# Kernel tuning notes

Measured on AMD Instinct MI355X. Metric: run time of the kernel, lower is better.

The kernel has to match this reference:

```python
import jax, jax.numpy as jnp
import numpy as np

BUCKET = 32   # bucket_size hard-coded in module
HEADS = 8
LN_EPS = 1e-5
SELF_ATTN_VALUE = -5e4  # TOKEN_SELF_ATTN_VALUE from reformer-pytorch


def _layer_norm(x, g, b):
    m = jnp.mean(x, axis=-1, keepdims=True)
    v = jnp.mean((x - m) ** 2, axis=-1, keepdims=True)
    return (x - m) / jnp.sqrt(v + LN_EPS) * g + b


def _lsh_attention(qk, v, rot):
    # qk, v: (B=b*h, T, Dh); rot: (Dh, n_buckets//2); n_hashes = 1
    B, T, D = qk.shape
    n_buckets = T // BUCKET
    # hash: random rotations, argmax over [r, -r]
    r = jnp.einsum('btf,fi->bti', qk, rot)                 # (B, T, n_buckets//2)
    r = jnp.concatenate([r, -r], axis=-1)                  # (B, T, n_buckets)
    buckets = jnp.argmax(r, axis=-1)                       # (B, T) int
    t = jnp.arange(T)
    key = buckets * T + t                                  # unique sort key
    sticker = jnp.argsort(key, axis=-1)                    # (B, T) permutation
    undo = jnp.argsort(sticker, axis=-1)
    sqk = jnp.take_along_axis(qk, sticker[..., None], axis=1)
    sv = jnp.take_along_axis(v, sticker[..., None], axis=1)
    # chunk into n_buckets chunks of size BUCKET
    bq_t = sticker.reshape(B, n_buckets, BUCKET)
    bq = sqk.reshape(B, n_buckets, BUCKET, D)
    bv = sv.reshape(B, n_buckets, BUCKET, D)
    nrm = jnp.sqrt(jnp.sum(bq * bq, axis=-1, keepdims=True))
    bk = bq / jnp.maximum(nrm, 1e-12)                      # shared-QK: keys are unit-norm queries
    def look_one_back(xx):
        return jnp.concatenate([xx, jnp.roll(xx, 1, axis=1)], axis=2)
    bk = look_one_back(bk)
    bvv = look_one_back(bv)
    bkv_t = look_one_back(bq_t)
    dots = jnp.einsum('bcie,bcje->bcij', bq, bk) * (D ** -0.5)  # (B, C, 32, 64)
    self_mask = bq_t[:, :, :, None] == bkv_t[:, :, None, :]
    dots = jnp.where(self_mask, SELF_ATTN_VALUE, dots)
    attn = jax.nn.softmax(dots, axis=-1)
    bo = jnp.einsum('bcij,bcje->bcie', attn, bvv)
    so = bo.reshape(B, T, D)
    return jnp.take_along_axis(so, undo[..., None], axis=1)   # unsort (n_hashes=1 -> probs=1)


def _lsh_self_attention(h, w_qk, w_v, w_out, b_out, rot):
    b, t, d = h.shape
    dh = d // HEADS
    qk = (h @ w_qk).reshape(b, t, HEADS, dh).transpose(0, 2, 1, 3).reshape(b * HEADS, t, dh)
    vv = (h @ w_v).reshape(b, t, HEADS, dh).transpose(0, 2, 1, 3).reshape(b * HEADS, t, dh)
    o = _lsh_attention(qk, vv, rot)
    o = o.reshape(b, HEADS, t, dh).transpose(0, 2, 1, 3).reshape(b, t, d)
    return o @ w_out + b_out


def setup_inputs() -> dict:
    key = jax.random.key(0)
    ks = jax.random.split(key, 8)
    B, T, D, F = 8, 4096, 512, 2048
    dh, nb = D // HEADS, T // BUCKET
    s = 0.02
    return {
        'x': jax.random.normal(ks[0], (B, T, D), jnp.float32),
        'w_qk': jax.random.normal(ks[1], (D, D), jnp.float32) * s,
        'w_v': jax.random.normal(ks[2], (D, D), jnp.float32) * s,
        'w_out': jax.random.normal(ks[3], (D, D), jnp.float32) * s,
        'b_out': jnp.zeros((D,), jnp.float32),
        'ln1_g': jnp.ones((D,), jnp.float32),
        'ln1_b': jnp.zeros((D,), jnp.float32),
        'w_ff1': jax.random.normal(ks[4], (D, F), jnp.float32) * s,
        'b_ff1': jnp.zeros((F,), jnp.float32),
        'w_ff2': jax.random.normal(ks[5], (F, D), jnp.float32) * s,
        'b_ff2': jnp.zeros((D,), jnp.float32),
        'ln2_g': jnp.ones((D,), jnp.float32),
        'ln2_b': jnp.zeros((D,), jnp.float32),
        'rotations': jax.random.normal(ks[6], (dh, nb // 2), jnp.float32),
    }


def reference(x, w_qk, w_v, w_out, b_out, ln1_g, ln1_b, w_ff1, b_ff1,
              w_ff2, b_ff2, ln2_g, ln2_b, rotations):
    # y1 = x + Attn(LN1(x)); y2 = x + FFN(LN2(y1)); out = mean(y1, y2)
    h1 = _layer_norm(x, ln1_g, ln1_b)
    y1 = x + _lsh_self_attention(h1, w_qk, w_v, w_out, b_out, rotations)
    h2 = _layer_norm(y1, ln2_g, ln2_b)
    ffn = jax.nn.relu(h2 @ w_ff1 + b_ff1) @ w_ff2 + b_ff2
    y2 = x + ffn
    return 0.5 * (y1 + y2)
```

## Files before the change

### kernel.cpp

```cpp
#include <hip/hip_runtime.h>
#include <stdint.h>

typedef _Float16 f16;
typedef _Float16 f16x8 __attribute__((ext_vector_type(8)));
typedef float    f32x4 __attribute__((ext_vector_type(4)));
typedef unsigned long long u64;

__device__ __forceinline__ void gload16(const void* g, void* l) {
  __builtin_amdgcn_global_load_lds(
      (__attribute__((address_space(1))) void*)g,
      (__attribute__((address_space(3))) void*)l, 16, 0, 0);
}

#define MFMA_QUAD(q, af) \
  _Pragma("unroll") for (int m2 = 0; m2 < 2; ++m2) \
  _Pragma("unroll") for (int nt = 0; nt < 4; ++nt) \
  _Pragma("unroll") for (int kk = 0; kk < 2; ++kk) \
    acc[(q)*2 + m2][nt] = __builtin_amdgcn_mfma_f32_16x16x32_f16( \
        af[m2][kk], bf[nt][kk], acc[(q)*2 + m2][nt], 0, 0, 0);

#define RD_A(dst, abase, q2) \
  _Pragma("unroll") for (int m2 = 0; m2 < 2; ++m2) \
  _Pragma("unroll") for (int kk = 0; kk < 2; ++kk) { \
    const int lr = (q2)*32 + m2*16 + l15; \
    dst[m2][kk] = *(const f16x8*)&abase[lr*64 + (((kk*4 + l4) ^ (lr & 7)) << 3)]; }

#define RD_B(bbase) \
  _Pragma("unroll") for (int nt = 0; nt < 4; ++nt) \
  _Pragma("unroll") for (int kk = 0; kk < 2; ++kk) { \
    const int lr = brow + nt*16 + l15; \
    bf[nt][kk] = *(const f16x8*)&bbase[lr*64 + (((kk*4 + l4) ^ (lr & 7)) << 3)]; }

#define PH_PRE() \
  __builtin_amdgcn_s_barrier(); \
  asm volatile("s_waitcnt lgkmcnt(0)" ::: "memory"); \
  __builtin_amdgcn_sched_barrier(0); \
  __builtin_amdgcn_s_setprio(1);

#define PH_POST() \
  __builtin_amdgcn_s_setprio(0); \
  __builtin_amdgcn_s_barrier(); \
  __builtin_amdgcn_sched_barrier(0);

template<int EPI>
__global__ __launch_bounds__(512, 2)
void gemm256(const f16* __restrict__ A, int lda,
             const f16* __restrict__ Bt, int ldb,
             int K, int N,
             float* __restrict__ outf, f16* __restrict__ outh,
             f16* __restrict__ outh2,
             const float* __restrict__ bias,
             const float* __restrict__ add1)
{
  __shared__ __align__(16) f16 lds[65536];
  const int tid = threadIdx.x, lane = tid & 63;
  const int wid = tid >> 6;
  const int wm = wid >> 2, wn = wid & 3;
  const int l15 = lane & 15, l4 = lane >> 4;

  const int gx = gridDim.x;
  int lid = blockIdx.y * gx + blockIdx.x;
  const int cpx = (gx * gridDim.y) >> 3;
  lid = (lid & 7) * cpx + (lid >> 3);
  const long bm0 = (long)(lid / gx) * 256;
  const long bn0 = (long)(lid % gx) * 256;

  const int rs = tid >> 3, cs = tid & 7;
  const int cg = cs ^ (rs & 7);
  const int nkt = K >> 6;
  const int nmask = nkt - 1;

  auto stageA = [&](int d, int half, int kt) {
    f16* dst = &lds[(d * 4 + half) * 8192];
    const long kb = (long)kt * 64 + cg * 8;
    const f16* src = A + (bm0 + half * 128) * lda + kb;
#pragma unroll
    for (int rr = 0; rr < 2; ++rr) {
      const int row = rs + rr * 64;
      gload16(src + (long)row * lda, dst + row * 64 + cs * 8);
    }
  };
  auto stageB = [&](int d, int half, int kt) {
    f16* dst = &lds[(d * 4 + 2 + half) * 8192];
    const long kb = (long)kt * 64 + cg * 8;
    const f16* src = Bt + (bn0 + half * 128) * ldb + kb;
#pragma unroll
    for (int rr = 0; rr < 2; ++rr) {
      const int row = rs + rr * 64;
      gload16(src + (long)row * ldb, dst + row * 64 + cs * 8);
    }
  };

  const f16* aBase0 = &lds[(0 + wm) * 8192];
  const f16* aBase1 = &lds[(4 + wm) * 8192];
  const f16* bBase0 = &lds[(2 + (wn >> 1)) * 8192];
  const f16* bBase1 = &lds[(6 + (wn >> 1)) * 8192];
  const int brow = (wn & 1) * 64;

  f32x4 acc[8][4];
#pragma unroll
  for (int i = 0; i < 8; ++i)
#pragma unroll
    for (int j = 0; j < 4; ++j) acc[i][j] = f32x4{0.f, 0.f, 0.f, 0.f};
  f16x8 bf[4][2], afA[2][2], afB[2][2];

  stageB(0, 0, 0); stageB(0, 1, 0); stageA(0, 0, 0); stageA(0, 1, 0);
  asm volatile("s_waitcnt vmcnt(4)" ::: "memory");
  stageB(1, 0, 1); stageB(1, 1, 1); stageA(1, 0, 1);
  asm volatile("s_waitcnt vmcnt(6)" ::: "memory");
  __builtin_amdgcn_s_barrier();
  __builtin_amdgcn_sched_barrier(0);

  for (int j = 0; j < nkt; j += 2) {
    const int t2 = (j + 2) & nmask, t3 = (j + 3) & nmask;
    RD_B(bBase0); RD_A(afA, aBase0, 0);
    stageA(1, 1, (j + 1) & nmask);
    asm volatile("s_waitcnt lgkmcnt(8)" ::: "memory");
    PH_PRE(); MFMA_QUAD(0, afA); PH_POST();
    RD_A(afB, aBase0, 1); RD_A(afA, aBase0, 2);
    stageB(0, 0, t2);
    PH_PRE(); MFMA_QUAD(1, afB); PH_POST();
    RD_A(afB, aBase0, 3);
    stageB(0, 1, t2);
    PH_PRE(); MFMA_QUAD(2, afA); PH_POST();
    stageA(0, 0, t2);
    asm volatile("s_waitcnt vmcnt(6)" ::: "memory");
    PH_PRE(); MFMA_QUAD(3, afB); PH_POST();
    RD_B(bBase1); RD_A(afA, aBase1, 0);
    stageA(0, 1, t2);
    asm volatile("s_waitcnt lgkmcnt(8)" ::: "memory");
    PH_PRE(); MFMA_QUAD(0, afA); PH_POST();
    RD_A(afB, aBase1, 1); RD_A(afA, aBase1, 2);
    stageB(1, 0, t3);
    PH_PRE(); MFMA_QUAD(1, afB); PH_POST();
    RD_A(afB, aBase1, 3);
    stageB(1, 1, t3);
    PH_PRE(); MFMA_QUAD(2, afA); PH_POST();
    stageA(1, 0, t3);
    asm volatile("s_waitcnt vmcnt(6)" ::: "memory");
    PH_PRE(); MFMA_QUAD(3, afB); PH_POST();
  }
  asm volatile("s_waitcnt vmcnt(0)" ::: "memory");

#pragma unroll
  for (int mt = 0; mt < 8; ++mt)
#pragma unroll
    for (int nt = 0; nt < 4; ++nt)
#pragma unroll
      for (int r = 0; r < 4; ++r) {
        const long grow = bm0 + wm * 128 + mt * 16 + l4 * 4 + r;
        const long gcol = bn0 + wn * 64 + nt * 16 + l15;
        const float c = acc[mt][nt][r];
        if constexpr (EPI == 12) {
          const long idx = grow * (long)N + gcol;
          outf[idx] = c + bias[gcol] + add1[idx];
        } else if constexpr (EPI == 13) {
          const long idx = grow * (long)N + gcol;
          outh[idx] = (f16)fmaxf(c + bias[gcol], 0.f);
        } else if constexpr (EPI == 17) {
          const int bb = (int)(grow >> 12), tt = (int)(grow & 4095);
          const int hcol = (int)(bn0 >> 6) + wn;
          const int is_v = hcol >> 3, h = hcol & 7;
          f16* base = is_v ? outh2 : outh;
          base[(((long)bb * 8 + h) * 4096 + tt) * 64 + nt * 16 + l15] = (f16)c;
        }
      }
}

__global__ __launch_bounds__(512)
void gemm8_ffn2(const f16* __restrict__ A,
                const f16* __restrict__ Bt,
                const f16* __restrict__ sxyh,
                const float* __restrict__ bias,
                float* __restrict__ outf)
{
  __shared__ __align__(16) f16 sA[128 * 64];
  __shared__ __align__(16) f16 sB[128 * 64];
  const int tid  = threadIdx.x;
  const int lane = tid & 63;
  const int wv   = tid >> 6;
  const int wm   = wv >> 2, wn = wv & 3;
  const int l15  = lane & 15, l4 = lane >> 4;

  const int gx = gridDim.x;
  int lid = blockIdx.y * gx + blockIdx.x;
  const int cpx = (gx * gridDim.y) >> 3;
  lid = (lid & 7) * cpx + (lid >> 3);
  const long bm0 = (long)(lid / gx) * 128;
  const long bn0 = (long)(lid % gx) * 128;

  f32x4 acc[4][2];
#pragma unroll
  for (int i = 0; i < 4; ++i)
#pragma unroll
    for (int j = 0; j < 2; ++j) acc[i][j] = f32x4{0.f, 0.f, 0.f, 0.f};

  const int rs = tid >> 3;
  const int cs = tid & 7;
  const int cg = cs ^ (rs & 7);

  for (int kt = 0; kt < 32; ++kt) {
    __syncthreads();
    const long ka = (long)kt * 64 + cg * 8;
#pragma unroll
    for (int rd = 0; rd < 2; ++rd) {
      const int row = rs + rd * 64;
      gload16(A + (bm0 + row) * 2048 + ka, &sA[row * 64 + cs * 8]);
    }
#pragma unroll
    for (int rd = 0; rd < 2; ++rd) {
      const int row = rs + rd * 64;
      gload16(Bt + (bn0 + row) * 2048 + ka, &sB[row * 64 + cs * 8]);
    }
    __syncthreads();
#pragma unroll
    for (int kk = 0; kk < 2; ++kk) {
      f16x8 af[4], bfr[2];
#pragma unroll
      for (int mt = 0; mt < 4; ++mt) {
        const int row = wm * 64 + mt * 16 + l15;
        const int c = kk * 4 + l4;
        af[mt] = *(const f16x8*)&sA[row * 64 + ((c ^ (row & 7)) << 3)];
      }
#pragma unroll
      for (int nt = 0; nt < 2; ++nt) {
        const int row = wn * 32 + nt * 16 + l15;
        const int c = kk * 4 + l4;
        bfr[nt] = *(const f16x8*)&sB[row * 64 + ((c ^ (row & 7)) << 3)];
      }
#pragma unroll
      for (int mt = 0; mt < 4; ++mt)
#pragma unroll
        for (int nt = 0; nt < 2; ++nt)
          acc[mt][nt] = __builtin_amdgcn_mfma_f32_16x16x32_f16(af[mt], bfr[nt], acc[mt][nt], 0, 0, 0);
    }
  }

#pragma unroll
  for (int mt = 0; mt < 4; ++mt)
#pragma unroll
    for (int nt = 0; nt < 2; ++nt)
#pragma unroll
      for (int r = 0; r < 4; ++r) {
        const long grow = bm0 + wm * 64 + mt * 16 + l4 * 4 + r;
        const long gcol = bn0 + wn * 32 + nt * 16 + l15;
        const long idx  = grow * 512 + gcol;
        outf[idx] = (float)sxyh[idx] + 0.5f * (acc[mt][nt][r] + bias[gcol]);
      }
}

__global__ __launch_bounds__(256)
void ln_kernel(const float* __restrict__ in, const float* __restrict__ gam,
               const float* __restrict__ bet, f16* __restrict__ out,
               int ldo, int split, const float* __restrict__ xin,
               f16* __restrict__ sxy)
{
  const long row = (long)blockIdx.x * 4 + (threadIdx.x >> 6);
  const int lane = threadIdx.x & 63;
  const float4* p = (const float4*)(in + row * 512);
  const float4 a = p[lane * 2], b = p[lane * 2 + 1];
  float xv[8] = {a.x, a.y, a.z, a.w, b.x, b.y, b.z, b.w};
  float s = 0.f;
#pragma unroll
  for (int i = 0; i < 8; ++i) s += xv[i];
#pragma unroll
  for (int m = 32; m; m >>= 1) s += __shfl_xor(s, m);
  const float mean = s * (1.f / 512.f);
  float vs = 0.f;
#pragma unroll
  for (int i = 0; i < 8; ++i) { const float d = xv[i] - mean; vs += d * d; }
#pragma unroll
  for (int m = 32; m; m >>= 1) vs += __shfl_xor(vs, m);
  const float rstd = 1.f / sqrtf(vs * (1.f / 512.f) + 1e-5f);
  const float4* gp = (const float4*)gam;
  const float4* bp = (const float4*)bet;
  const float4 g0 = gp[lane * 2], g1 = gp[lane * 2 + 1];
  const float4 b0 = bp[lane * 2], b1 = bp[lane * 2 + 1];
  const float gg[8] = {g0.x, g0.y, g0.z, g0.w, g1.x, g1.y, g1.z, g1.w};
  const float bb[8] = {b0.x, b0.y, b0.z, b0.w, b1.x, b1.y, b1.z, b1.w};
  f16x8 vh, vl;
#pragma unroll
  for (int i = 0; i < 8; ++i) {
    const float y = (xv[i] - mean) * rstd * gg[i] + bb[i];
    const f16 hi = (f16)y;
    vh[i] = hi;
    vl[i] = (f16)((y - (float)hi) * 64.f);
  }
  f16* o = out + row * ldo + lane * 8;
  *(f16x8*)o = vh;
  if (split) *(f16x8*)(o + 512) = vl;
  if (sxy) {
    const float4* xp = (const float4*)(xin + row * 512);
    const float4 x0 = xp[lane * 2], x1 = xp[lane * 2 + 1];
    const float xx[8] = {x0.x, x0.y, x0.z, x0.w, x1.x, x1.y, x1.z, x1.w};
    f16x8 vsx;
#pragma unroll
    for (int i = 0; i < 8; ++i) vsx[i] = (f16)(0.5f * (xv[i] + xx[i]));
    *(f16x8*)(sxy + row * 512 + lane * 8) = vsx;
  }
}

__global__ __launch_bounds__(256)
void transpose_f16(const float* __restrict__ src, f16* __restrict__ dst, int K, int N)
{
  __shared__ float tile[32][33];
  const int tx = threadIdx.x & 31, ty = threadIdx.x >> 5;
  const long k0 = (long)blockIdx.y * 32, n0 = (long)blockIdx.x * 32;
#pragma unroll
  for (int i = 0; i < 4; ++i)
    tile[ty + i * 8][tx] = src[(k0 + ty + i * 8) * N + n0 + tx];
  __syncthreads();
#pragma unroll
  for (int i = 0; i < 4; ++i)
    dst[(n0 + ty + i * 8) * K + k0 + tx] = (f16)tile[tx][ty + i * 8];
}

__global__ __launch_bounds__(256)
void whash_f32(const float* __restrict__ wqk, const float* __restrict__ rot,
               float* __restrict__ WrT, f16* __restrict__ rotTh)
{
  if (blockIdx.x == 0 && blockIdx.y == 0) {
    for (int idx = threadIdx.x; idx < 4096; idx += 256) {
      const int d = idx >> 6, i = idx & 63;
      rotTh[i * 64 + d] = (f16)rot[idx];
    }
  }
  const int kk = blockIdx.x;
  const int n  = blockIdx.y * 256 + threadIdx.x;
  const int h = n >> 6, i = n & 63;
  float s = 0.f;
  for (int d = 0; d < 64; ++d)
    s += wqk[kk * 512 + h * 64 + d] * rot[d * 64 + i];
  WrT[(long)n * 512 + kk] = s;
}

__global__ __launch_bounds__(256)
void rhash4_kernel(const f16* __restrict__ gqk, const f16* __restrict__ rotTh,
                   int* __restrict__ buckets)
{
  const int tid = threadIdx.x, lane = tid & 63, w = tid >> 6;
  const int bh = blockIdx.x >> 5, tb = blockIdx.x & 31;
  const int t0 = tb * 128;
  const int l15 = lane & 15, l4 = lane >> 4;

  f16x8 br[2][4];
#pragma unroll
  for (int kk = 0; kk < 2; ++kk)
#pragma unroll
    for (int nt = 0; nt < 4; ++nt)
      br[kk][nt] = *(const f16x8*)&rotTh[(nt * 16 + l15) * 64 + kk * 32 + l4 * 8];

  const f16* gqb = gqk + ((long)bh * 4096 + t0) * 64;
  f16x8 aq[2][2];
#pragma unroll
  for (int kk = 0; kk < 2; ++kk)
#pragma unroll
    for (int mt = 0; mt < 2; ++mt)
      aq[kk][mt] = *(const f16x8*)&gqb[(long)(w * 32 + mt * 16 + l15) * 64 + kk * 32 + l4 * 8];

  f32x4 acc[2][4];
#pragma unroll
  for (int i = 0; i < 2; ++i)
#pragma unroll
    for (int j = 0; j < 4; ++j) acc[i][j] = f32x4{0.f, 0.f, 0.f, 0.f};
#pragma unroll
  for (int kk = 0; kk < 2; ++kk)
#pragma unroll
    for (int mt = 0; mt < 2; ++mt)
#pragma unroll
      for (int nt = 0; nt < 4; ++nt)
        acc[mt][nt] = __builtin_amdgcn_mfma_f32_16x16x32_f16(aq[kk][mt], br[kk][nt], acc[mt][nt], 0, 0, 0);

#pragma unroll
  for (int mt = 0; mt < 2; ++mt)
#pragma unroll
    for (int r = 0; r < 4; ++r) {
      const float v0 = acc[mt][0][r], v1 = acc[mt][1][r];
      const float v2 = acc[mt][2][r], v3 = acc[mt][3][r];
      unsigned int k0 = (__float_as_uint(fabsf(v0)) & ~63u) | (unsigned int)(63 - l15);
      unsigned int k1 = (__float_as_uint(fabsf(v1)) & ~63u) | (unsigned int)(47 - l15);
      unsigned int k2 = (__float_as_uint(fabsf(v2)) & ~63u) | (unsigned int)(31 - l15);
      unsigned int k3 = (__float_as_uint(fabsf(v3)) & ~63u) | (unsigned int)(15 - l15);
      float ss = v0 * v0 + v1 * v1 + v2 * v2 + v3 * v3;
#pragma unroll
      for (int m = 1; m < 16; m <<= 1) ss += __shfl_xor(ss, m);

      unsigned int mk = max(max(k0, k1), max(k2, k3));
#pragma unroll
      for (int m = 1; m < 16; m <<= 1) mk = max(mk, (unsigned int)__shfl_xor((int)mk, m));
      const unsigned int key1 = mk;
      const int col1 = 63 - (int)(key1 & 63u);
      const float m1f = __uint_as_float(key1 & ~63u);
      const int nt1 = col1 >> 4;
      const float vsel = (nt1 == 0) ? v0 : (nt1 == 1) ? v1 : (nt1 == 2) ? v2 : v3;
      const bool owner = (col1 & 15) == l15;
      const u64 bal = __ballot(owner && (vsel < 0.f));
      const int neg = (int)((bal >> (l4 * 16 + (col1 & 15))) & 1ull);
      const int bucket = col1 + (neg << 6);
      if (owner) {
        if (nt1 == 0) k0 = 0; else if (nt1 == 1) k1 = 0;
        else if (nt1 == 2) k2 = 0; else k3 = 0;
      }
      mk = max(max(k0, k1), max(k2, k3));
#pragma unroll
      for (int m = 1; m < 16; m <<= 1) mk = max(mk, (unsigned int)__shfl_xor((int)mk, m));
      const int col2 = 63 - (int)(mk & 63u);
      const float m2f = __uint_as_float(mk & ~63u);
      {
        const int nt2 = col2 >> 4;
        if ((col2 & 15) == l15) {
          if (nt2 == 0) k0 = 0; else if (nt2 == 1) k1 = 0;
          else if (nt2 == 2) k2 = 0; else k3 = 0;
        }
      }
      mk = max(max(k0, k1), max(k2, k3));
#pragma unroll
      for (int m = 1; m < 16; m <<= 1) mk = max(mk, (unsigned int)__shfl_xor((int)mk, m));
      const int col3 = 63 - (int)(mk & 63u);

      if (l15 == 0) {
        const int row = w * 32 + mt * 16 + l4 * 4 + r;
        const int bht = bh * 4096 + t0 + row;
        const float margin = m1f - m2f;
        const float rms = sqrtf(ss * (1.f / 64.f));
        const int flag = (margin < 0.015f * rms) ? 1 : 0;
        buckets[bht] = bucket | (col2 << 8) | (col3 << 16) | (flag << 24);
      }
    }
}

__global__ __launch_bounds__(256)
void fixup2_kernel(const f16* __restrict__ hsplit, const float* __restrict__ WrT,
                   int* __restrict__ buckets)
{
  const int wid = (blockIdx.x * 256 + threadIdx.x) >> 6;
  const int lane = threadIdx.x & 63;
  for (int batch = 0; batch < 4; ++batch) {
    const int base = wid * 256 + batch * 64;
    const int packed = buckets[base + lane];
    u64 bal = __ballot((packed >> 24) & 1);
    while (bal) {
      const int i = (int)__ffsll((long long)bal) - 1;
      bal &= bal - 1;
      const int row = base + i;
      const int pk = __shfl(packed, i);
      const int h = (row >> 12) & 7;
      const long hrow = (long)(row >> 15) * 4096 + (row & 4095);
      const f16* hp = hsplit + hrow * 1024 + lane * 8;
      const f16x8 hi = *(const f16x8*)hp;
      const f16x8 lo = *(const f16x8*)(hp + 512);
      float h1[8];
#pragma unroll
      for (int k = 0; k < 8; ++k) h1[k] = (float)hi[k] + (float)lo[k] * 0.015625f;
      const int cols[3] = { pk & 63, (pk >> 8) & 63, (pk >> 16) & 63 };
      float best = -1e30f; int bi = 999;
#pragma unroll
      for (int c = 0; c < 3; ++c) {
        const int cc = cols[c];
        const float* wp = WrT + ((long)(h * 64 + cc)) * 512 + lane * 8;
        const float4 w0 = *(const float4*)wp;
        const float4 w1 = *(const float4*)(wp + 4);
        float s = h1[0] * w0.x + h1[1] * w0.y + h1[2] * w0.z + h1[3] * w0.w
                + h1[4] * w1.x + h1[5] * w1.y + h1[6] * w1.z + h1[7] * w1.w;
#pragma unroll
        for (int m = 32; m; m >>= 1) s += __shfl_xor(s, m);
        if (s > best || (s == best && cc < bi)) { best = s; bi = cc; }
        const float ns = -s; const int ni = 64 + cc;
        if (ns > best || (ns == best && ni < bi)) { best = ns; bi = ni; }
      }
      if (lane == 0) buckets[row] = bi;
    }
  }
}

__global__ __launch_bounds__(256)
void sort_kernel(const int* __restrict__ buckets, int* __restrict__ sticker)
{
  __shared__ int bkt[4096];
  __shared__ unsigned int cnts[64][128];
  __shared__ unsigned char rnk[4096];
  __shared__ int tot[128];
  __shared__ int base[128];
  const int bh = blockIdx.x;
  const int tid = threadIdx.x;
  const int lane = tid & 63, wv = tid >> 6;

  for (int i = tid; i < 4096; i += 256) bkt[i] = buckets[(long)bh * 4096 + i] & 127;
  for (int i = tid; i < 64 * 128; i += 256) ((unsigned int*)cnts)[i] = 0u;
  __syncthreads();

  for (int it = 0; it < 16; ++it) {
    const int c = wv * 16 + it;
    const int t = c * 64 + lane;
    const int b = bkt[t];
    unsigned long long m = ~0ull;
#pragma unroll
    for (int k = 0; k < 7; ++k) {
      const bool bit = (b >> k) & 1;
      const unsigned long long bal = __ballot(bit);
      m &= bit ? bal : ~bal;
    }
    const int rk = (int)__popcll(m & ((1ull << lane) - 1ull));
    rnk[t] = (unsigned char)rk;
    if (rk == 0) cnts[c][b] = (unsigned int)__popcll(m);
  }
  __syncthreads();

  if (tid < 128) {
    unsigned int run = 0;
    for (int c = 0; c < 64; ++c) {
      const unsigned int x = cnts[c][tid];
      cnts[c][tid] = run;
      run += x;
    }
    tot[tid] = (int)run;
  }
  __syncthreads();
  if (tid == 0) {
    int run = 0;
    for (int b = 0; b < 128; ++b) { base[b] = run; run += tot[b]; }
  }
  __syncthreads();

  for (int it = 0; it < 16; ++it) {
    const int c = wv * 16 + it;
    const int t = c * 64 + lane;
    const int b = bkt[t];
    const int pos = base[b] + (int)cnts[c][b] + (int)rnk[t];
    sticker[(long)bh * 4096 + pos] = t;
  }
}

__global__ __launch_bounds__(256)
void attn2_kernel(const f16* __restrict__ gqk, const f16* __restrict__ gv,
                  const int* __restrict__ sticker, f16* __restrict__ o)
{
  __shared__ __align__(16) f16 sqk[160 * 64];
  __shared__ __align__(16) f16 sVT[64 * 168];
  __shared__ __align__(16) f16 sP[4][32 * 72];
  __shared__ float rnorm[160];
  __shared__ int st[160];

  const int tid = threadIdx.x, lane = tid & 63, w = tid >> 6;
  const int cg = blockIdx.x, bh = blockIdx.y;
  const int b = bh >> 3, h = bh & 7;
  const int p0 = cg * 128 - 32;
  const int l15 = lane & 15, l4 = lane >> 4;

  if (tid < 160) st[tid] = sticker[(long)bh * 4096 + ((p0 + tid) & 4095)] & 4095;
  __syncthreads();

  const f16* gqb = gqk + (long)bh * 4096 * 64;
#pragma unroll
  for (int it = 0; it < 5; ++it) {
    const int idx = it * 256 + tid;
    const int row = idx >> 3, ch = idx & 7;
    const int gsrc = ch ^ (row & 7);
    gload16(gqb + (long)st[row] * 64 + gsrc * 8, &sqk[idx * 8]);
  }

  const f16* gvb = gv + (long)bh * 4096 * 64;
  f16x8 va[5];
#pragma unroll
  for (int i = 0; i < 5; ++i) {
    const int row = w * 40 + i * 8 + (lane >> 3);
    va[i] = *(const f16x8*)&gvb[(long)st[row] * 64 + (lane & 7) * 8];
  }
#pragma unroll
  for (int i = 0; i < 5; ++i) {
    const int row = w * 40 + i * 8 + (lane >> 3);
    const int d0 = (lane & 7) * 8;
#pragma unroll
    for (int e = 0; e < 8; ++e) sVT[(d0 + e) * 168 + row] = va[i][e];
  }
  __syncthreads();

  if (tid < 160) {
    float s = 0.f;
#pragma unroll
    for (int g = 0; g < 8; ++g) {
      const f16x8 v = *(const f16x8*)&sqk[tid * 64 + ((g ^ (tid & 7)) << 3)];
#pragma unroll
      for (int e = 0; e < 8; ++e) { const float f = (float)v[e]; s += f * f; }
    }
    rnorm[tid] = 1.f / fmaxf(sqrtf(s), 1e-12f);
  }
  __syncthreads();

  f32x4 acc[2][4];
#pragma unroll
  for (int i = 0; i < 2; ++i)
#pragma unroll
    for (int j = 0; j < 4; ++j) acc[i][j] = f32x4{0.f, 0.f, 0.f, 0.f};

#pragma unroll
  for (int kk = 0; kk < 2; ++kk) {
    f16x8 aq[2], bk[4];
#pragma unroll
    for (int mt = 0; mt < 2; ++mt) {
      const int row = 32 + w * 32 + mt * 16 + l15;
      const int g = kk * 4 + l4;
      aq[mt] = *(const f16x8*)&sqk[row * 64 + ((g ^ (row & 7)) << 3)];
    }
#pragma unroll
    for (int nt = 0; nt < 4; ++nt) {
      const int row = w * 32 + nt * 16 + l15;
      const int g = kk * 4 + l4;
      bk[nt] = *(const f16x8*)&sqk[row * 64 + ((g ^ (row & 7)) << 3)];
    }
#pragma unroll
    for (int mt = 0; mt < 2; ++mt)
#pragma unroll
      for (int nt = 0; nt < 4; ++nt)
        acc[mt][nt] = __builtin_amdgcn_mfma_f32_16x16x32_f16(aq[mt], bk[nt], acc[mt][nt], 0, 0, 0);
  }

  float rn[4];
#pragma unroll
  for (int nt = 0; nt < 4; ++nt) rn[nt] = rnorm[w * 32 + nt * 16 + l15];

  float pinv[2][4];
#pragma unroll
  for (int mt = 0; mt < 2; ++mt)
#pragma unroll
    for (int r = 0; r < 4; ++r) {
      const int row_i = mt * 16 + l4 * 4 + r;
      float mx = -1e30f;
#pragma unroll
      for (int nt = 0; nt < 4; ++nt) {
        float v = acc[mt][nt][r] * 0.125f * rn[nt];
        if (nt * 16 + l15 == row_i + 32) v = -5e4f;
        acc[mt][nt][r] = v;
        mx = fmaxf(mx, v);
      }
#pragma unroll
      for (int m = 8; m; m >>= 1) mx = fmaxf(mx, __shfl_xor(mx, m));
      float ssum = 0.f;
#pragma unroll
      for (int nt = 0; nt < 4; ++nt) {
        const float pe = expf(acc[mt][nt][r] - mx);
        ssum += pe;
        sP[w][row_i * 72 + nt * 16 + l15] = (f16)pe;
      }
#pragma unroll
      for (int m = 8; m; m >>= 1) ssum += __shfl_xor(ssum, m);
      pinv[mt][r] = 1.f / ssum;
    }
  __syncthreads();

  f32x4 pacc[2][4];
#pragma unroll
  for (int i = 0; i < 2; ++i)
#pragma unroll
    for (int j = 0; j < 4; ++j) pacc[i][j] = f32x4{0.f, 0.f, 0.f, 0.f};

#pragma unroll
  for (int kk = 0; kk < 2; ++kk) {
    f16x8 ap[2], bv[4];
#pragma unroll
    for (int mt = 0; mt < 2; ++mt)
      ap[mt] = *(const f16x8*)&sP[w][(mt * 16 + l15) * 72 + kk * 32 + l4 * 8];
#pragma unroll
    for (int nt = 0; nt < 4; ++nt)
      bv[nt] = *(const f16x8*)&sVT[(nt * 16 + l15) * 168 + w * 32 + kk * 32 + l4 * 8];
#pragma unroll
    for (int mt = 0; mt < 2; ++mt)
#pragma unroll
      for (int nt = 0; nt < 4; ++nt)
        pacc[mt][nt] = __builtin_amdgcn_mfma_f32_16x16x32_f16(ap[mt], bv[nt], pacc[mt][nt], 0, 0, 0);
  }

  const long ob = (long)b * 4096 * 512 + h * 64;
#pragma unroll
  for (int mt = 0; mt < 2; ++mt)
#pragma unroll
    for (int r = 0; r < 4; ++r) {
      const int row_i = mt * 16 + l4 * 4 + r;
      const long t = st[32 + w * 32 + row_i];
      const float sc = pinv[mt][r];
#pragma unroll
      for (int nt = 0; nt < 4; ++nt)
        o[ob + t * 512 + nt * 16 + l15] = (f16)(pacc[mt][nt][r] * sc);
    }
}

extern "C" void kernel_launch(void* const* d_in, const int* in_sizes, int n_in,
                              void* d_out, int out_size, void* d_ws, size_t ws_size,
                              hipStream_t stream)
{
  const float* x     = (const float*)d_in[0];
  const float* w_qk  = (const float*)d_in[1];
  const float* w_v   = (const float*)d_in[2];
  const float* w_out = (const float*)d_in[3];
  const float* b_out = (const float*)d_in[4];
  const float* ln1g  = (const float*)d_in[5];
  const float* ln1b  = (const float*)d_in[6];
  const float* w_ff1 = (const float*)d_in[7];
  const float* b_ff1 = (const float*)d_in[8];
  const float* w_ff2 = (const float*)d_in[9];
  const float* b_ff2 = (const float*)d_in[10];
  const float* ln2g  = (const float*)d_in[11];
  const float* ln2b  = (const float*)d_in[12];
  const float* rot   = (const float*)d_in[13];
  float* out = (float*)d_out;

  char* ws = (char*)d_ws;
  f16* hsplit = (f16*)ws;
  f16* o_buf  = (f16*)ws;
  f16* sxy    = (f16*)ws;
  f16* h2     = (f16*)(ws + 33554432);
  f16* gqk    = (f16*)(ws + 67108864);
  f16* gv     = (f16*)(ws + 100663296);
  f16* abuf   = (f16*)(ws + 67108864);
  char* W0 = ws + 134217728;
  f16* wqkvT = (f16*)W0;
  f16* woutT = (f16*)(W0 + 1048576);
  f16* wff1T = (f16*)(W0 + 1572864);
  f16* wff2T = (f16*)(W0 + 3670016);
  float* WrT = (float*)(W0 + 5767168);
  int* buckets = (int*)(W0 + 6815744);
  int* sticker = (int*)(W0 + 7864320);
  f16* rotTh   = (f16*)(W0 + 8912896);

  const dim3 b256(256);
  const dim3 b512(512);
  transpose_f16<<<dim3(16, 16), b256, 0, stream>>>(w_qk,  wqkvT,             512, 512);
  transpose_f16<<<dim3(16, 16), b256, 0, stream>>>(w_v,   wqkvT + 512 * 512, 512, 512);
  transpose_f16<<<dim3(16, 16), b256, 0, stream>>>(w_out, woutT,             512, 512);
  transpose_f16<<<dim3(64, 16), b256, 0, stream>>>(w_ff1, wff1T,             512, 2048);
  transpose_f16<<<dim3(16, 64), b256, 0, stream>>>(w_ff2, wff2T,             2048, 512);
  whash_f32<<<dim3(512, 2), b256, 0, stream>>>(w_qk, rot, WrT, rotTh);
  ln_kernel<<<dim3(8192), b256, 0, stream>>>(x, ln1g, ln1b, hsplit, 1024, 1, nullptr, nullptr);
  gemm256<17><<<dim3(4, 128), b512, 0, stream>>>(hsplit, 1024, wqkvT, 512, 512, 1024,
      nullptr, gqk, gv, nullptr, nullptr);
  rhash4_kernel<<<dim3(2048), b256, 0, stream>>>(gqk, rotTh, buckets);
  fixup2_kernel<<<dim3(256), b256, 0, stream>>>(hsplit, WrT, buckets);
  sort_kernel<<<dim3(64), b256, 0, stream>>>(buckets, sticker);
  attn2_kernel<<<dim3(32, 64), b256, 0, stream>>>(gqk, gv, sticker, o_buf);
  gemm256<12><<<dim3(2, 128), b512, 0, stream>>>(o_buf, 512, woutT, 512, 512, 512,
      out, nullptr, nullptr, b_out, x);
  ln_kernel<<<dim3(8192), b256, 0, stream>>>(out, ln2g, ln2b, h2, 512, 0, x, sxy);
  for (int c = 0; c < 2; ++c) {
    const long roff = (long)c * 16384;
    gemm256<13><<<dim3(8, 64), b512, 0, stream>>>(h2 + roff * 512, 512, wff1T, 512,
        512, 2048, nullptr, abuf, nullptr, b_ff1, nullptr);
    gemm8_ffn2<<<dim3(4, 128), b512, 0, stream>>>(abuf, wff2T, sxy + roff * 512,
        b_ff2, out + roff * 512);
  }
}
```

Baseline: 468.4 us.

## Rewrite FFN2 GEMM with 256x128 tiles and double-buffered async LDS pipeline

Replaces the simple 128x128 single-buffered FFN2 GEMM with a 256x128 tile kernel. Each warp now computes 64x64 instead of 64x32, which raises reuse of data loaded into LDS. The new kernel double-buffers the K-loop with global_load_lds prefetches two steps ahead and uses explicit waitcnt, barrier and phase macros to interleave MFMAs with LDS reads. It cuts per-iteration barriers and halves the grid. The costs are higher register pressure, 96KB of LDS per block, and fewer blocks (256) to fill the CUs. The loop relies on hand-tuned vmcnt/lgkmcnt counts and on the PH_PRE/PH_POST macros defined elsewhere.

```diff
diff --git a/kernel.cpp b/kernel.cpp
--- a/kernel.cpp
+++ b/kernel.cpp
@@ -167,84 +167,122 @@
       }
 }
 
-__global__ __launch_bounds__(512)
-void gemm8_ffn2(const f16* __restrict__ A,
-                const f16* __restrict__ Bt,
-                const f16* __restrict__ sxyh,
-                const float* __restrict__ bias,
-                float* __restrict__ outf)
-{
-  __shared__ __align__(16) f16 sA[128 * 64];
-  __shared__ __align__(16) f16 sB[128 * 64];
-  const int tid  = threadIdx.x;
-  const int lane = tid & 63;
-  const int wv   = tid >> 6;
-  const int wm   = wv >> 2, wn = wv & 3;
-  const int l15  = lane & 15, l4 = lane >> 4;
+#define RD2_B(bbase) \
+  _Pragma("unroll") for (int nt = 0; nt < 4; ++nt) \
+  _Pragma("unroll") for (int kk = 0; kk < 2; ++kk) { \
+    const int lr = brow + nt*16 + l15; \
+    bf[nt][kk] = *(const f16x8*)&bbase[lr*64 + (((kk*4 + l4) ^ (lr & 7)) << 3)]; }
+
+#define RD2_A(dst, abase, mt) \
+  _Pragma("unroll") for (int kk = 0; kk < 2; ++kk) { \
+    const int lr = arow + (mt)*16 + l15; \
+    dst[kk] = *(const f16x8*)&abase[lr*64 + (((kk*4 + l4) ^ (lr & 7)) << 3)]; }
+
+#define MFMA_Q1(mt, af) \
+  _Pragma("unroll") for (int nt = 0; nt < 4; ++nt) \
+  _Pragma("unroll") for (int kk = 0; kk < 2; ++kk) \
+    acc[mt][nt] = __builtin_amdgcn_mfma_f32_16x16x32_f16( \
+        af[kk], bf[nt][kk], acc[mt][nt], 0, 0, 0);
+
+__global__ __launch_bounds__(512, 2)
+void ffn2_8ph(const f16* __restrict__ A, const f16* __restrict__ Bt,
+              const f16* __restrict__ sxyh, const float* __restrict__ bias,
+              float* __restrict__ outf)
+{
+  __shared__ __align__(16) f16 lds[49152];
+  const int tid = threadIdx.x, lane = tid & 63;
+  const int wid = tid >> 6;
+  const int wm = wid >> 1, wn = wid & 1;
+  const int l15 = lane & 15, l4 = lane >> 4;
 
   const int gx = gridDim.x;
   int lid = blockIdx.y * gx + blockIdx.x;
   const int cpx = (gx * gridDim.y) >> 3;
   lid = (lid & 7) * cpx + (lid >> 3);
-  const long bm0 = (long)(lid / gx) * 128;
+  const long bm0 = (long)(lid / gx) * 256;
   const long bn0 = (long)(lid % gx) * 128;
 
-  f32x4 acc[4][2];
+  const int rs = tid >> 3, cs = tid & 7;
+  const int cg = cs ^ (rs & 7);
+  const int nmask = 31;
+
+  auto stageA = [&](int d, int half, int kt) {
+    f16* dst = &lds[(d * 3 + half) * 8192];
+    const long kb = (long)kt * 64 + cg * 8;
+    const f16* src = A + (bm0 + half * 128) * 2048 + kb;
+#pragma unroll
+    for (int rr = 0; rr < 2; ++rr) {
+      const int row = rs + rr * 64;
+      gload16(src + (long)row * 2048, dst + row * 64 + cs * 8);
+    }
+  };
+  auto stageB = [&](int d, int kt) {
+    f16* dst = &lds[(d * 3 + 2) * 8192];
+    const long kb = (long)kt * 64 + cg * 8;
+    const f16* src = Bt + bn0 * 2048 + kb;
+#pragma unroll
+    for (int rr = 0; rr < 2; ++rr) {
+      const int row = rs + rr * 64;
+      gload16(src + (long)row * 2048, dst + row * 64 + cs * 8);
+    }
+  };
+
+  const f16* aBase0 = &lds[(0 + (wm >> 1)) * 8192];
+  const f16* aBase1 = &lds[(3 + (wm >> 1)) * 8192];
+  const f16* bBase0 = &lds[2 * 8192];
+  const f16* bBase1 = &lds[5 * 8192];
+  const int arow = (wm & 1) * 64;
+  const int brow = wn * 64;
+
+  f32x4 acc[4][4];
 #pragma unroll
   for (int i = 0; i < 4; ++i)
 #pragma unroll
-    for (int j = 0; j < 2; ++j) acc[i][j] = f32x4{0.f, 0.f, 0.f, 0.f};
-
-  const int rs = tid >> 3;
-  const int cs = tid & 7;
-  const int cg = cs ^ (rs & 7);
-
-  for (int kt = 0; kt < 32; ++kt) {
-    __syncthreads();
-    const long ka = (long)kt * 64 + cg * 8;
-#pragma unroll
-    for (int rd = 0; rd < 2; ++rd) {
-      const int row = rs + rd * 64;
-      gload16(A + (bm0 + row) * 2048 + ka, &sA[row * 64 + cs * 8]);
-    }
-#pragma unroll
-    for (int rd = 0; rd < 2; ++rd) {
-      const int row = rs + rd * 64;
-      gload16(Bt + (bn0 + row) * 2048 + ka, &sB[row * 64 + cs * 8]);
-    }
-    __syncthreads();
-#pragma unroll
-    for (int kk = 0; kk < 2; ++kk) {
-      f16x8 af[4], bfr[2];
-#pragma unroll
-      for (int mt = 0; mt < 4; ++mt) {
-        const int row = wm * 64 + mt * 16 + l15;
-        const int c = kk * 4 + l4;
-        af[mt] = *(const f16x8*)&sA[row * 64 + ((c ^ (row & 7)) << 3)];
-      }
-#pragma unroll
-      for (int nt = 0; nt < 2; ++nt) {
-        const int row = wn * 32 + nt * 16 + l15;
-        const int c = kk * 4 + l4;
-        bfr[nt] = *(const f16x8*)&sB[row * 64 + ((c ^ (row & 7)) << 3)];
-      }
-#pragma unroll
-      for (int mt = 0; mt < 4; ++mt)
-#pragma unroll
-        for (int nt = 0; nt < 2; ++nt)
-          acc[mt][nt] = __builtin_amdgcn_mfma_f32_16x16x32_f16(af[mt], bfr[nt], acc[mt][nt], 0, 0, 0);
-    }
-  }
+    for (int j = 0; j < 4; ++j) acc[i][j] = f32x4{0.f, 0.f, 0.f, 0.f};
+  f16x8 bf[4][2], afA[2], afB[2];
+
+  stageB(0, 0); stageA(0, 0, 0); stageA(0, 1, 0);
+  stageB(1, 1); stageA(1, 0, 1); stageA(1, 1, 1);
+  asm volatile("s_waitcnt vmcnt(6)" ::: "memory");
+  __builtin_amdgcn_s_barrier();
+  __builtin_amdgcn_sched_barrier(0);
+
+  for (int j = 0; j < 32; j += 2) {
+    const int t2 = (j + 2) & nmask, t3 = (j + 3) & nmask;
+    RD2_B(bBase0); RD2_A(afA, aBase0, 0);
+    asm volatile("s_waitcnt lgkmcnt(8)" ::: "memory");
+    PH_PRE(); MFMA_Q1(0, afA); PH_POST();
+    RD2_A(afB, aBase0, 1); RD2_A(afA, aBase0, 2);
+    stageB(0, t2);
+    PH_PRE(); MFMA_Q1(1, afB); PH_POST();
+    RD2_A(afB, aBase0, 3);
+    PH_PRE(); MFMA_Q1(2, afA); PH_POST();
+    stageA(0, 0, t2); stageA(0, 1, t2);
+    asm volatile("s_waitcnt vmcnt(6)" ::: "memory");
+    PH_PRE(); MFMA_Q1(3, afB); PH_POST();
+    RD2_B(bBase1); RD2_A(afA, aBase1, 0);
+    asm volatile("s_waitcnt lgkmcnt(8)" ::: "memory");
+    PH_PRE(); MFMA_Q1(0, afA); PH_POST();
+    RD2_A(afB, aBase1, 1); RD2_A(afA, aBase1, 2);
+    stageB(1, t3);
+    PH_PRE(); MFMA_Q1(1, afB); PH_POST();
+    RD2_A(afB, aBase1, 3);
+    PH_PRE(); MFMA_Q1(2, afA); PH_POST();
+    stageA(1, 0, t3); stageA(1, 1, t3);
+    asm volatile("s_waitcnt vmcnt(6)" ::: "memory");
+    PH_PRE(); MFMA_Q1(3, afB); PH_POST();
+  }
+  asm volatile("s_waitcnt vmcnt(0)" ::: "memory");
 
 #pragma unroll
   for (int mt = 0; mt < 4; ++mt)
 #pragma unroll
-    for (int nt = 0; nt < 2; ++nt)
+    for (int nt = 0; nt < 4; ++nt)
 #pragma unroll
       for (int r = 0; r < 4; ++r) {
         const long grow = bm0 + wm * 64 + mt * 16 + l4 * 4 + r;
-        const long gcol = bn0 + wn * 32 + nt * 16 + l15;
-        const long idx  = grow * 512 + gcol;
+        const long gcol = bn0 + wn * 64 + nt * 16 + l15;
+        const long idx = grow * 512 + gcol;
         outf[idx] = (float)sxyh[idx] + 0.5f * (acc[mt][nt][r] + bias[gcol]);
       }
 }
@@ -744,7 +782,7 @@
     const long roff = (long)c * 16384;
     gemm256<13><<<dim3(8, 64), b512, 0, stream>>>(h2 + roff * 512, 512, wff1T, 512,
         512, 2048, nullptr, abuf, nullptr, b_ff1, nullptr);
-    gemm8_ffn2<<<dim3(4, 128), b512, 0, stream>>>(abuf, wff2T, sxy + roff * 512,
+    ffn2_8ph<<<dim3(4, 64), b512, 0, stream>>>(abuf, wff2T, sxy + roff * 512,
         b_ff2, out + roff * 512);
   }
 }
```

Result: no change. 459.4 us (-1.9%).
